# Kernel optimization log

Measured on AMD Instinct MI355X. Metric: run time of the kernel, lower is better.

Reference implementation:

```python
import jax, jax.numpy as jnp
import numpy as np

DIM = 1024
HEADS = 16
HEAD_DIM = DIM // HEADS
SCALE = HEAD_DIM ** -0.5


def setup_inputs() -> dict:
    key = jax.random.key(0)
    ks = jax.random.split(key, 6)
    B, N, C = 2, 2048, DIM
    s = C ** -0.5
    return {
        "x": jax.random.normal(ks[0], (B, N, C), dtype=jnp.float32),
        "Wq": jax.random.normal(ks[1], (C, C), dtype=jnp.float32) * s,
        "Wk": jax.random.normal(ks[2], (C, C), dtype=jnp.float32) * s,
        "Wv": jax.random.normal(ks[3], (C, C), dtype=jnp.float32) * s,
        "Wo": jax.random.normal(ks[4], (C, C), dtype=jnp.float32) * s,
        "bo": jax.random.normal(ks[5], (C,), dtype=jnp.float32) * 0.02,
    }


def reference(x, Wq, Wk, Wv, Wo, bo):
    B, N, C = x.shape
    H, D = HEADS, HEAD_DIM
    # q/k/v linears (no bias), reshape to [B, H, N, D]
    q = (x @ Wq.T).reshape(B, N, H, D).transpose(0, 2, 1, 3)
    k = (x @ Wk.T).reshape(B, N, H, D).transpose(0, 2, 1, 3)
    v = (x @ Wv.T).reshape(B, N, H, D).transpose(0, 2, 1, 3)
    attn = jnp.einsum("bhnd,bhmd->bhnm", q, k) * SCALE  # [B,H,N,N]
    attn = jax.nn.softmax(attn, axis=-1)
    out = jnp.einsum("bhnm,bhmd->bhnd", attn, v)  # [B,H,N,D]
    out = out.transpose(0, 2, 1, 3).reshape(B, N, C)
    out = out @ Wo.T + bo  # proj (dropout p=0 in eval -> identity)
    return out
```

## Files before the change

kernel.cpp:

```cpp
#include <hip/hip_runtime.h>
#include <stdint.h>

typedef __attribute__((ext_vector_type(8))) _Float16 half8;
typedef __attribute__((ext_vector_type(8))) unsigned short ushort8;
typedef __attribute__((ext_vector_type(4))) float f32x4;
typedef unsigned short u16;

#define AS1C(p) ((const __attribute__((address_space(1))) void*)(p))
#define AS3(p)  ((__attribute__((address_space(3))) void*)(p))

__device__ __forceinline__ f32x4 mfma_k32(half8 a, half8 b, f32x4 c) {
  return __builtin_amdgcn_mfma_f32_16x16x32_f16(a, b, c, 0, 0, 0);
}
__device__ __forceinline__ u16 f2h(float f) {
  return __builtin_bit_cast(u16, (_Float16)f);
}
__device__ __forceinline__ float fexp2(float x) {
  return __builtin_amdgcn_exp2f(x);
}
__device__ __forceinline__ unsigned int pk2h(float a, float b) {
  return __builtin_bit_cast(unsigned int, __builtin_amdgcn_cvt_pkrtz(a, b));
}
__device__ __forceinline__ int fsz(int r) {
  return (((r & 3) | (((r >> 3) & 1) << 2)) << 4);
}

__global__ __launch_bounds__(256) void k_convert(
    const float* __restrict__ x, const float* __restrict__ wq,
    const float* __restrict__ wk, const float* __restrict__ wv,
    const float* __restrict__ wo,
    u16* __restrict__ xb, u16* __restrict__ wqkvb, u16* __restrict__ wob) {
  size_t t = (size_t)blockIdx.x * 256 + threadIdx.x;
  size_t e = t * 8;
  const float* src;
  u16* dst;
  if (e < 4194304u)      { src = x  + e;            dst = xb    + e; }
  else if (e < 5242880u) { src = wq + (e-4194304u); dst = wqkvb + (e-4194304u); }
  else if (e < 6291456u) { src = wk + (e-5242880u); dst = wqkvb + (e-4194304u); }
  else if (e < 7340032u) { src = wv + (e-6291456u); dst = wqkvb + (e-4194304u); }
  else                   { src = wo + (e-7340032u); dst = wob   + (e-7340032u); }
  float4 a = *(const float4*)src;
  float4 b = *(const float4*)(src + 4);
  ushort8 o;
  o[0]=f2h(a.x); o[1]=f2h(a.y); o[2]=f2h(a.z); o[3]=f2h(a.w);
  o[4]=f2h(b.x); o[5]=f2h(b.y); o[6]=f2h(b.z); o[7]=f2h(b.w);
  *(ushort8*)dst = o;
}

__device__ __forceinline__ void gemm_core(
    const u16* __restrict__ Ag, const u16* __restrict__ Bg,
    int row0, int col0, char* lAc, char* lBc, f32x4 acc[4][4]) {
  const int tid = threadIdx.x;
  const int w = tid >> 6, lane = tid & 63;
  const int wm = (w >> 1) * 64, wn = (w & 1) * 64;
  const int l15 = lane & 15, l4 = lane >> 4;
#pragma unroll
  for (int i = 0; i < 4; ++i)
#pragma unroll
    for (int j = 0; j < 4; ++j) acc[i][j] = (f32x4){0.f, 0.f, 0.f, 0.f};

  const int lrow = lane >> 2;
  const int lcb  = (lane & 3) << 4;
  const char* Abase = (const char*)Ag + (size_t)row0 * 2048;
  const char* Bbase = (const char*)Bg + (size_t)col0 * 2048;

  auto stage = [&](int buf, int kt) {
#pragma unroll
    for (int i = 0; i < 2; ++i) {
      int c = w + 4 * i;
      int r = c * 16 + lrow;
      __builtin_amdgcn_global_load_lds(AS1C(Abase + (size_t)r * 2048 + kt * 64 + lcb),
                                       AS3(lAc + buf * 8192 + c * 1024), 16, 0, 0);
      __builtin_amdgcn_global_load_lds(AS1C(Bbase + (size_t)r * 2048 + kt * 64 + lcb),
                                       AS3(lBc + buf * 8192 + c * 1024), 16, 0, 0);
    }
  };

  stage(0, 0);
  __syncthreads();
  int cur = 0;
  for (int kt = 0; kt < 32; ++kt) {
    if (kt < 31) stage(cur ^ 1, kt + 1);
    const char* A = lAc + cur * 8192;
    const char* B = lBc + cur * 8192;
    half8 af[4], bf[4];
#pragma unroll
    for (int mi = 0; mi < 4; ++mi)
      af[mi] = *(const half8*)(A + (wm + mi * 16 + l15) * 64 + (l4 << 4));
#pragma unroll
    for (int ni = 0; ni < 4; ++ni)
      bf[ni] = *(const half8*)(B + (wn + ni * 16 + l15) * 64 + (l4 << 4));
#pragma unroll
    for (int mi = 0; mi < 4; ++mi)
#pragma unroll
      for (int ni = 0; ni < 4; ++ni)
        acc[mi][ni] = mfma_k32(af[mi], bf[ni], acc[mi][ni]);
    __syncthreads();
    cur ^= 1;
  }
}

__global__ __launch_bounds__(256) void k_gemm_qkv(
    const u16* __restrict__ xb, const u16* __restrict__ wqkvb,
    u16* __restrict__ qk, u16* __restrict__ vt) {
  __shared__ u16 lA[2 * 4096];
  __shared__ u16 lB[2 * 4096];
  f32x4 acc[4][4];
  const int lid = blockIdx.x;
  const int xcd = lid & 7, idx = lid >> 3;
  const int pr = idx / 12, pc = idx % 12;
  const int row0 = (((xcd & 3) << 3) + pr) << 7;
  const int col0 = ((xcd >> 2) * 12 + pc) << 7;
  gemm_core(xb, wqkvb, row0, col0, (char*)lA, (char*)lB, acc);

  const int w = threadIdx.x >> 6, lane = threadIdx.x & 63;
  const int l15 = lane & 15, l4 = lane >> 4;
  const int rbase = row0 + (w >> 1) * 64 + (l4 << 2);
  const int cbase = col0 + (w & 1) * 64 + l15;
  const bool isQ = (col0 < 1024);
  const bool isV = (col0 >= 2048);
#pragma unroll
  for (int mi = 0; mi < 4; ++mi) {
#pragma unroll
    for (int ni = 0; ni < 4; ++ni) {
      const int col = cbase + ni * 16;
      if (!isV) {
#pragma unroll
        for (int r = 0; r < 4; ++r) {
          int row = rbase + mi * 16 + r;
          float v = acc[mi][ni][r];
          if (isQ) v *= 0.18033688f;
          qk[(size_t)row * 2048 + col] = f2h(v);
        }
      } else {
        const int jj = col - 2048;
        const int h = jj >> 6, d = jj & 63;
        const int row = rbase + mi * 16;
        const int b = row >> 11, n = row & 2047;
        u16 pk[4];
#pragma unroll
        for (int r = 0; r < 4; ++r) pk[r] = f2h(acc[mi][ni][r]);
        *(uint2*)&vt[(size_t)(((b << 4) + h) * 64 + d) * 2048 + n] = *(uint2*)pk;
      }
    }
  }
}

__global__ __launch_bounds__(256) void k_attn(
    const u16* __restrict__ qk, const u16* __restrict__ vt, u16* __restrict__ ao) {
  __shared__ u16 KV[4][4096];
  char* L = (char*)&KV[0][0];
  const int lid = blockIdx.x;
  const int xcd = lid & 7, sub = lid >> 3;
  const int bh = (xcd << 2) + (sub >> 5);
  const int qt = sub & 31;
  const int b = bh >> 4, h = bh & 15;
  const int w = threadIdx.x >> 6, lane = threadIdx.x & 63;
  const int l15 = lane & 15, l4 = lane >> 4;

  const int qrow = (b << 11) + (qt << 6) + (w << 4) + l15;
  half8 qf[2];
  qf[0] = *(const half8*)(qk + (size_t)qrow * 2048 + h * 64 + (l4 << 3));
  qf[1] = *(const half8*)(qk + (size_t)qrow * 2048 + h * 64 + 32 + (l4 << 3));

  half8 vones8;
#pragma unroll
  for (int j = 0; j < 8; ++j) vones8[j] = (_Float16)1.0f;

  const int lrow = lane >> 3;
  const int lcb  = (lane & 7) << 4;
  const char* Kbase = (const char*)qk + (size_t)(b << 11) * 4096 + 2048 + h * 128;
  const char* Vbase = (const char*)vt + (size_t)(bh * 64) * 4096;

  const int rr0 = (w << 3) + lrow;
  const int sc0 = lcb ^ fsz(rr0);
  const char* kg0 = Kbase + (size_t)rr0 * 4096 + sc0;
  const char* kg1 = kg0 + 131072;
  const char* vg0 = Vbase + (size_t)rr0 * 4096 + sc0;
  const char* vg1 = vg0 + 131072;
  const int kd0 = w * 1024, kd1 = (w + 4) * 1024;

  const int keybase = ((l15 >> 2) << 3) + (l15 & 3);
  const int kswz = fsz(keybase);
  const int vswz = (((l15 & 3) | (((l15 >> 3) & 1) << 2)) << 4);
  int koff[8], voff[8];
#pragma unroll
  for (int nt = 0; nt < 4; ++nt) {
    const int key = keybase + ((nt & 1) << 2) + ((nt >> 1) << 5);
    koff[2 * nt]     = key * 128 + ((l4 << 4) ^ kswz);
    koff[2 * nt + 1] = key * 128 + (((l4 << 4) + 64) ^ kswz);
  }
#pragma unroll
  for (int dt = 0; dt < 4; ++dt) {
    const int d = dt * 16 + l15;
    voff[2 * dt]     = 16384 + d * 128 + ((l4 << 4) ^ vswz);
    voff[2 * dt + 1] = 16384 + d * 128 + (((l4 << 4) + 64) ^ vswz);
  }

  float m_run = -1e30f;
  f32x4 acc_o[4];
  f32x4 acc_l = (f32x4){0.f, 0.f, 0.f, 0.f};
#pragma unroll
  for (int dt = 0; dt < 4; ++dt) acc_o[dt] = (f32x4){0.f, 0.f, 0.f, 0.f};

  auto stage = [&](int buf) {
    __builtin_amdgcn_global_load_lds(AS1C(kg0), AS3(L + buf * 8192 + kd0), 16, 0, 0);
    __builtin_amdgcn_global_load_lds(AS1C(kg1), AS3(L + buf * 8192 + kd1), 16, 0, 0);
    __builtin_amdgcn_global_load_lds(AS1C(vg0), AS3(L + 16384 + buf * 8192 + kd0), 16, 0, 0);
    __builtin_amdgcn_global_load_lds(AS1C(vg1), AS3(L + 16384 + buf * 8192 + kd1), 16, 0, 0);
    kg0 += 262144; kg1 += 262144; vg0 += 128; vg1 += 128;
  };

  auto body = [&](int bu, bool do_stage) {
    if (do_stage) {
      stage(bu ^ 1);
      asm volatile("s_waitcnt vmcnt(4)" ::: "memory");
    } else {
      asm volatile("s_waitcnt vmcnt(0)" ::: "memory");
    }
    __builtin_amdgcn_s_barrier();
    __builtin_amdgcn_sched_barrier(0);
    const char* Lb = L + bu * 8192;

    f32x4 s[4];
    __builtin_amdgcn_s_setprio(1);
#pragma unroll
    for (int nt = 0; nt < 4; ++nt) {
      half8 k0 = *(const half8*)(Lb + koff[2 * nt]);
      half8 k1 = *(const half8*)(Lb + koff[2 * nt + 1]);
      f32x4 z = (f32x4){0.f, 0.f, 0.f, 0.f};
      z = mfma_k32(k0, qf[0], z);
      s[nt] = mfma_k32(k1, qf[1], z);
    }
    __builtin_amdgcn_s_setprio(0);

    float t0 = fmaxf(fmaxf(s[0][0], s[0][1]), s[0][2]);
    float t1 = fmaxf(fmaxf(s[0][3], s[1][0]), s[1][1]);
    float t2 = fmaxf(fmaxf(s[1][2], s[1][3]), s[2][0]);
    float t3 = fmaxf(fmaxf(s[2][1], s[2][2]), s[2][3]);
    float t4 = fmaxf(fmaxf(s[3][0], s[3][1]), s[3][2]);
    float tm = fmaxf(fmaxf(fmaxf(t0, t1), fmaxf(t2, t3)), fmaxf(t4, s[3][3]));

    const bool skip = __all(tm - m_run <= 8.f);
    float mnew = m_run;
    if (!skip) {
      tm = fmaxf(tm, __shfl_xor(tm, 16));
      tm = fmaxf(tm, __shfl_xor(tm, 32));
      mnew = fmaxf(m_run, tm);
      float alpha = fexp2(m_run - mnew);
      m_run = mnew;
#pragma unroll
      for (int dt = 0; dt < 4; ++dt)
#pragma unroll
        for (int r = 0; r < 4; ++r) acc_o[dt][r] *= alpha;
      acc_l[0] *= alpha;
    }

    half8 pb[2];
#pragma unroll
    for (int p = 0; p < 2; ++p) {
      uint4 pk;
      pk.x = pk2h(fexp2(s[2*p][0] - mnew),   fexp2(s[2*p][1] - mnew));
      pk.y = pk2h(fexp2(s[2*p][2] - mnew),   fexp2(s[2*p][3] - mnew));
      pk.z = pk2h(fexp2(s[2*p+1][0] - mnew), fexp2(s[2*p+1][1] - mnew));
      pk.w = pk2h(fexp2(s[2*p+1][2] - mnew), fexp2(s[2*p+1][3] - mnew));
      pb[p] = __builtin_bit_cast(half8, pk);
    }

    __builtin_amdgcn_s_setprio(1);
#pragma unroll
    for (int dt = 0; dt < 4; ++dt) {
      half8 v0 = *(const half8*)(Lb + voff[2 * dt]);
      half8 v1 = *(const half8*)(Lb + voff[2 * dt + 1]);
      acc_o[dt] = mfma_k32(v0, pb[0], acc_o[dt]);
      acc_o[dt] = mfma_k32(v1, pb[1], acc_o[dt]);
    }
    acc_l = mfma_k32(vones8, pb[0], acc_l);
    acc_l = mfma_k32(vones8, pb[1], acc_l);
    __builtin_amdgcn_s_setprio(0);

    __builtin_amdgcn_s_barrier();
  };

  stage(0);
  for (int k2 = 0; k2 < 16; ++k2) {
    body(0, true);
    body(1, k2 < 15);
  }

  const float inv = __builtin_amdgcn_rcpf(acc_l[0]);
  const size_t rowbase = ((size_t)(b << 11) + (qt << 6) + (w << 4) + l15) * 1024 + h * 64;
#pragma unroll
  for (int dt = 0; dt < 4; ++dt) {
    uint2 o;
    o.x = pk2h(acc_o[dt][0] * inv, acc_o[dt][1] * inv);
    o.y = pk2h(acc_o[dt][2] * inv, acc_o[dt][3] * inv);
    *(uint2*)&ao[rowbase + dt * 16 + (l4 << 2)] = o;
  }
}

__global__ __launch_bounds__(256) void k_gemm_proj(
    const u16* __restrict__ aob, const u16* __restrict__ wob,
    const float* __restrict__ bo, float* __restrict__ out) {
  __shared__ u16 lA[2 * 4096];
  __shared__ u16 lB[2 * 4096];
  f32x4 acc[4][4];
  const int lid = blockIdx.x;
  const int xcd = lid & 7, idx = lid >> 3;
  const int row0 = ((xcd << 2) + (idx >> 3)) << 7;
  const int col0 = (idx & 7) << 7;
  gemm_core(aob, wob, row0, col0, (char*)lA, (char*)lB, acc);

  const int w = threadIdx.x >> 6, lane = threadIdx.x & 63;
  const int l15 = lane & 15, l4 = lane >> 4;
  const int rbase = row0 + (w >> 1) * 64 + (l4 << 2);
  const int cbase = col0 + (w & 1) * 64 + l15;
#pragma unroll
  for (int mi = 0; mi < 4; ++mi) {
#pragma unroll
    for (int ni = 0; ni < 4; ++ni) {
      const int col = cbase + ni * 16;
      const float bb = bo[col];
#pragma unroll
      for (int r = 0; r < 4; ++r) {
        const int row = rbase + mi * 16 + r;
        out[(size_t)row * 1024 + col] = acc[mi][ni][r] + bb;
      }
    }
  }
}

extern "C" void kernel_launch(void* const* d_in, const int* in_sizes, int n_in,
                              void* d_out, int out_size, void* d_ws, size_t ws_size,
                              hipStream_t stream) {
  const float* x  = (const float*)d_in[0];
  const float* wq = (const float*)d_in[1];
  const float* wk = (const float*)d_in[2];
  const float* wv = (const float*)d_in[3];
  const float* wo = (const float*)d_in[4];
  const float* bo = (const float*)d_in[5];
  float* out = (float*)d_out;

  char* ws = (char*)d_ws;
  u16* xb    = (u16*)(ws);
  u16* wqkvb = (u16*)(ws + 8388608);
  u16* wob   = (u16*)(ws + 14680064);
  u16* qkb   = (u16*)(ws + 16777216);
  u16* vtb   = (u16*)(ws + 33554432);
  u16* aob   = (u16*)(ws + 41943040);

  k_convert<<<dim3(4096), dim3(256), 0, stream>>>(x, wq, wk, wv, wo, xb, wqkvb, wob);
  k_gemm_qkv<<<dim3(768), dim3(256), 0, stream>>>(xb, wqkvb, qkb, vtb);
  k_attn<<<dim3(1024), dim3(256), 0, stream>>>(qkb, vtb, aob);
  k_gemm_proj<<<dim3(256), dim3(256), 0, stream>>>(aob, wob, bo, out);
}
```

Before: 130.9 us.

## Triple-buffer LDS staging in GEMM and attention loops with one barrier per step

Switches the GEMM core and the attention KV loop from double to triple buffering. Loads run two tiles ahead, and each step uses a single vmcnt wait plus one barrier instead of two barriers. The goal is to hide global-to-LDS latency better and cut synchronization per iteration. LDS use grows by half, which can lower occupancy per CU.

```diff
diff --git a/kernel.cpp b/kernel.cpp
--- a/kernel.cpp
+++ b/kernel.cpp
@@ -8,6 +8,11 @@
 
 #define AS1C(p) ((const __attribute__((address_space(1))) void*)(p))
 #define AS3(p)  ((__attribute__((address_space(3))) void*)(p))
+
+#define PIPE_W4 do { asm volatile("s_waitcnt vmcnt(4)" ::: "memory"); \
+  __builtin_amdgcn_s_barrier(); __builtin_amdgcn_sched_barrier(0); } while (0)
+#define PIPE_W0 do { asm volatile("s_waitcnt vmcnt(0)" ::: "memory"); \
+  __builtin_amdgcn_s_barrier(); __builtin_amdgcn_sched_barrier(0); } while (0)
 
 __device__ __forceinline__ f32x4 mfma_k32(half8 a, half8 b, f32x4 c) {
   return __builtin_amdgcn_mfma_f32_16x16x32_f16(a, b, c, 0, 0, 0);
@@ -75,14 +80,9 @@
                                        AS3(lBc + buf * 8192 + c * 1024), 16, 0, 0);
     }
   };
-
-  stage(0, 0);
-  __syncthreads();
-  int cur = 0;
-  for (int kt = 0; kt < 32; ++kt) {
-    if (kt < 31) stage(cur ^ 1, kt + 1);
-    const char* A = lAc + cur * 8192;
-    const char* B = lBc + cur * 8192;
+  auto compute = [&](int buf) {
+    const char* A = lAc + buf * 8192;
+    const char* B = lBc + buf * 8192;
     half8 af[4], bf[4];
 #pragma unroll
     for (int mi = 0; mi < 4; ++mi)
@@ -95,16 +95,24 @@
 #pragma unroll
       for (int ni = 0; ni < 4; ++ni)
         acc[mi][ni] = mfma_k32(af[mi], bf[ni], acc[mi][ni]);
-    __syncthreads();
-    cur ^= 1;
-  }
+  };
+
+  stage(0, 0);
+  stage(1, 1);
+  for (int k3 = 0; k3 < 30; k3 += 3) {
+    PIPE_W4; stage(2, k3 + 2); compute(0);
+    PIPE_W4; stage(0, k3 + 3); compute(1);
+    PIPE_W4; stage(1, k3 + 4); compute(2);
+  }
+  PIPE_W4; compute(0);
+  PIPE_W0; compute(1);
 }
 
 __global__ __launch_bounds__(256) void k_gemm_qkv(
     const u16* __restrict__ xb, const u16* __restrict__ wqkvb,
     u16* __restrict__ qk, u16* __restrict__ vt) {
-  __shared__ u16 lA[2 * 4096];
-  __shared__ u16 lB[2 * 4096];
+  __shared__ u16 lA[3 * 4096];
+  __shared__ u16 lB[3 * 4096];
   f32x4 acc[4][4];
   const int lid = blockIdx.x;
   const int xcd = lid & 7, idx = lid >> 3;
@@ -148,7 +156,7 @@
 
 __global__ __launch_bounds__(256) void k_attn(
     const u16* __restrict__ qk, const u16* __restrict__ vt, u16* __restrict__ ao) {
-  __shared__ u16 KV[4][4096];
+  __shared__ u16 KV[6][4096];
   char* L = (char*)&KV[0][0];
   const int lid = blockIdx.x;
   const int xcd = lid & 7, sub = lid >> 3;
@@ -193,8 +201,8 @@
 #pragma unroll
   for (int dt = 0; dt < 4; ++dt) {
     const int d = dt * 16 + l15;
-    voff[2 * dt]     = 16384 + d * 128 + ((l4 << 4) ^ vswz);
-    voff[2 * dt + 1] = 16384 + d * 128 + (((l4 << 4) + 64) ^ vswz);
+    voff[2 * dt]     = 24576 + d * 128 + ((l4 << 4) ^ vswz);
+    voff[2 * dt + 1] = 24576 + d * 128 + (((l4 << 4) + 64) ^ vswz);
   }
 
   float m_run = -1e30f;
@@ -206,20 +214,12 @@
   auto stage = [&](int buf) {
     __builtin_amdgcn_global_load_lds(AS1C(kg0), AS3(L + buf * 8192 + kd0), 16, 0, 0);
     __builtin_amdgcn_global_load_lds(AS1C(kg1), AS3(L + buf * 8192 + kd1), 16, 0, 0);
-    __builtin_amdgcn_global_load_lds(AS1C(vg0), AS3(L + 16384 + buf * 8192 + kd0), 16, 0, 0);
-    __builtin_amdgcn_global_load_lds(AS1C(vg1), AS3(L + 16384 + buf * 8192 + kd1), 16, 0, 0);
+    __builtin_amdgcn_global_load_lds(AS1C(vg0), AS3(L + 24576 + buf * 8192 + kd0), 16, 0, 0);
+    __builtin_amdgcn_global_load_lds(AS1C(vg1), AS3(L + 24576 + buf * 8192 + kd1), 16, 0, 0);
     kg0 += 262144; kg1 += 262144; vg0 += 128; vg1 += 128;
   };
 
-  auto body = [&](int bu, bool do_stage) {
-    if (do_stage) {
-      stage(bu ^ 1);
-      asm volatile("s_waitcnt vmcnt(4)" ::: "memory");
-    } else {
-      asm volatile("s_waitcnt vmcnt(0)" ::: "memory");
-    }
-    __builtin_amdgcn_s_barrier();
-    __builtin_amdgcn_sched_barrier(0);
+  auto compute = [&](int bu) {
     const char* Lb = L + bu * 8192;
 
     f32x4 s[4];
@@ -278,15 +278,17 @@
     acc_l = mfma_k32(vones8, pb[0], acc_l);
     acc_l = mfma_k32(vones8, pb[1], acc_l);
     __builtin_amdgcn_s_setprio(0);
-
-    __builtin_amdgcn_s_barrier();
   };
 
   stage(0);
-  for (int k2 = 0; k2 < 16; ++k2) {
-    body(0, true);
-    body(1, k2 < 15);
-  }
+  stage(1);
+  for (int k3 = 0; k3 < 30; k3 += 3) {
+    PIPE_W4; stage(2); compute(0);
+    PIPE_W4; stage(0); compute(1);
+    PIPE_W4; stage(1); compute(2);
+  }
+  PIPE_W4; compute(0);
+  PIPE_W0; compute(1);
 
   const float inv = __builtin_amdgcn_rcpf(acc_l[0]);
   const size_t rowbase = ((size_t)(b << 11) + (qt << 6) + (w << 4) + l15) * 1024 + h * 64;
@@ -302,8 +304,8 @@
 __global__ __launch_bounds__(256) void k_gemm_proj(
     const u16* __restrict__ aob, const u16* __restrict__ wob,
     const float* __restrict__ bo, float* __restrict__ out) {
-  __shared__ u16 lA[2 * 4096];
-  __shared__ u16 lB[2 * 4096];
+  __shared__ u16 lA[3 * 4096];
+  __shared__ u16 lB[3 * 4096];
   f32x4 acc[4][4];
   const int lid = blockIdx.x;
   const int xcd = lid & 7, idx = lid >> 3;
```

Result: faster. 124.9 us (-4.6%).
